# Kernel tuning notes

Hardware: AMD Instinct MI355X
Metric: run time of the kernel (lower is better)

## Reference

```python
import jax, jax.numpy as jnp
import numpy as np

BN_EPS = 1e-5


def setup_inputs() -> dict:
    key = jax.random.key(0)
    ks = jax.random.split(key, 12)
    N, K, C_IN, C_OUT = 50000, 16, 128, 128
    C2 = 2 * C_OUT
    return {
        "features": jax.random.normal(ks[0], (N, C_IN), dtype=jnp.float32),
        "neighbor_idx": jax.random.randint(ks[1], (N, K), 0, N, dtype=jnp.int64),
        "W1": jax.random.normal(ks[2], (C_IN, C2), dtype=jnp.float32) * 0.05,
        "b1": jax.random.normal(ks[3], (C2,), dtype=jnp.float32) * 0.05,
        "gamma": jax.random.uniform(ks[4], (C2,), dtype=jnp.float32, minval=0.5, maxval=1.5),
        "beta": jax.random.normal(ks[5], (C2,), dtype=jnp.float32) * 0.05,
        "run_mean": jax.random.normal(ks[6], (C2,), dtype=jnp.float32) * 0.05,
        "run_var": jax.random.uniform(ks[7], (C2,), dtype=jnp.float32, minval=0.5, maxval=1.5),
        "Ws": jax.random.normal(ks[8], (C2, C2), dtype=jnp.float32) * 0.05,
        "Wm": jax.random.normal(ks[9], (C2, C_OUT), dtype=jnp.float32) * 0.05,
        "bm": jax.random.normal(ks[10], (C_OUT,), dtype=jnp.float32) * 0.05,
    }


def reference(features, neighbor_idx, W1, b1, gamma, beta, run_mean, run_var, Ws, Wm, bm):
    # mlp1: Linear + ReLU (no BN)
    x = jax.nn.relu(features @ W1 + b1)                     # (N, 2C)
    # gather_neighbour: irregular index_select
    g = x[neighbor_idx]                                     # (N, k, 2C)
    # BatchNorm1d over channel dim (inference semantics, running stats)
    inv = gamma * jax.lax.rsqrt(run_var + BN_EPS)
    g = (g - run_mean) * inv + beta                         # (N, k, 2C)
    # AttentivePooling: per-neighbor score linear (no bias), softmax over k
    scores = jax.nn.softmax(g @ Ws, axis=1)                 # (N, k, 2C)
    feat = jnp.sum(scores * g, axis=1)                      # (N, 2C)
    return feat @ Wm + bm                                   # (N, C_out)
```

## Files before the change

kernel.cpp:

```cpp
#include <hip/hip_runtime.h>
#include <cstddef>

#define C_IN  128
#define C2    256
#define C_OUT 128
#define KNBR  16

typedef unsigned short u16;
typedef __attribute__((ext_vector_type(8))) short bf16x8;
typedef __attribute__((ext_vector_type(8))) unsigned short u16x8;
typedef __attribute__((ext_vector_type(4))) float f32x4;

__device__ __forceinline__ float bf2f(u16 h) {
    return __uint_as_float(((unsigned int)h) << 16);
}
__device__ __forceinline__ u16 f2bf(float x) {
    unsigned int u = __float_as_uint(x);
    return (u16)((u + 0x7fffu + ((u >> 16) & 1u)) >> 16);
}

__global__ void prep_k(const float* __restrict__ W1, const float* __restrict__ Ws,
                       const float* __restrict__ Wm, u16* __restrict__ W1t,
                       u16* __restrict__ Wst, u16* __restrict__ Wmt)
{
    const int n = blockIdx.x, t = threadIdx.x;
    if (blockIdx.y == 0) {
        if (t < 128) W1t[n * 128 + t] = f2bf(W1[t * 256 + n]);
    } else if (blockIdx.y == 1) {
        Wst[n * 256 + t] = f2bf(Ws[t * 256 + n]);
    } else {
        if (n < 128) Wmt[n * 256 + t] = f2bf(Wm[t * 128 + n]);
    }
}


__global__ __launch_bounds__(256)
void mlp_k(const float* __restrict__ F, const u16* __restrict__ W1t,
           const u16* __restrict__ Wst,
           const float* __restrict__ bias, const float* __restrict__ gamma,
           const float* __restrict__ beta, const float* __restrict__ mean,
           const float* __restrict__ var,
           u16* __restrict__ packed, int N)
{
    __shared__ u16 As[64][136];
    __shared__ u16 Bs[128][72];
    __shared__ u16 xs[64][264];

    const int tid = threadIdx.x;
    const int w = tid >> 6, l = tid & 63, q = l >> 4, r = l & 15;
    const int wm = w & 1, wn = w >> 1;
    const int m0 = blockIdx.x * 64;

    #pragma unroll
    for (int i = 0; i < 8; i++) {
        int idx = tid + i * 256;
        int row = idx >> 5, c4 = (idx & 31) * 4;
        int gm = m0 + row;
        float4 v = make_float4(0.f, 0.f, 0.f, 0.f);
        if (gm < N) v = *(const float4*)(F + (size_t)gm * C_IN + c4);
        ushort4 h;
        h.x = f2bf(v.x); h.y = f2bf(v.y); h.z = f2bf(v.z); h.w = f2bf(v.w);
        *(ushort4*)&As[row][c4] = h;
    }

    #pragma unroll
    for (int nh = 0; nh < 2; nh++) {
        f32x4 acc[2][4] = {};
        #pragma unroll 1
        for (int k0 = 0; k0 < C_IN; k0 += 64) {
            __syncthreads();
            #pragma unroll
            for (int i = 0; i < 4; i++) {
                int idx = tid + i * 256;
                int row = idx >> 3, g = (idx & 7) * 8;
                *(uint4*)&Bs[row][g] = *(const uint4*)(
                    W1t + (size_t)(nh * 128 + row) * C_IN + k0 + g);
            }
            __syncthreads();
            #pragma unroll
            for (int h = 0; h < 2; h++) {
                bf16x8 af[2], bfr[4];
                #pragma unroll
                for (int i = 0; i < 2; i++)
                    af[i] = *(const bf16x8*)&As[wm * 32 + i * 16 + r][k0 + h * 32 + q * 8];
                #pragma unroll
                for (int j = 0; j < 4; j++)
                    bfr[j] = *(const bf16x8*)&Bs[wn * 64 + j * 16 + r][h * 32 + q * 8];
                #pragma unroll
                for (int i = 0; i < 2; i++)
                    #pragma unroll
                    for (int j = 0; j < 4; j++)
                        acc[i][j] = __builtin_amdgcn_mfma_f32_16x16x32_bf16(
                            af[i], bfr[j], acc[i][j], 0, 0, 0);
            }
        }
        #pragma unroll
        for (int j = 0; j < 4; j++) {
            const int ch = nh * 128 + wn * 64 + j * 16 + r;
            const float bi = bias[ch], be = beta[ch], mu = mean[ch];
            const float iv = gamma[ch] * rsqrtf(var[ch] + 1e-5f);
            #pragma unroll
            for (int i = 0; i < 2; i++) {
                const int mb = wm * 32 + i * 16 + q * 4;
                #pragma unroll
                for (int p = 0; p < 4; p++) {
                    float x = fmaxf(acc[i][j][p] + bi, 0.f);
                    x = (x - mu) * iv + be;
                    xs[mb + p][ch] = f2bf(x);
                }
            }
        }
    }
    __syncthreads();

    #pragma unroll
    for (int nh = 0; nh < 2; nh++) {
        f32x4 acc[2][4] = {};
        #pragma unroll 1
        for (int k0 = 0; k0 < C2; k0 += 64) {
            __syncthreads();
            #pragma unroll
            for (int i = 0; i < 4; i++) {
                int idx = tid + i * 256;
                int row = idx >> 3, g = (idx & 7) * 8;
                *(uint4*)&Bs[row][g] = *(const uint4*)(
                    Wst + (size_t)(nh * 128 + row) * C2 + k0 + g);
            }
            __syncthreads();
            #pragma unroll
            for (int h = 0; h < 2; h++) {
                bf16x8 af[2], bfr[4];
                #pragma unroll
                for (int i = 0; i < 2; i++)
                    af[i] = *(const bf16x8*)&xs[wm * 32 + i * 16 + r][k0 + h * 32 + q * 8];
                #pragma unroll
                for (int j = 0; j < 4; j++)
                    bfr[j] = *(const bf16x8*)&Bs[wn * 64 + j * 16 + r][h * 32 + q * 8];
                #pragma unroll
                for (int i = 0; i < 2; i++)
                    #pragma unroll
                    for (int j = 0; j < 4; j++)
                        acc[i][j] = __builtin_amdgcn_mfma_f32_16x16x32_bf16(
                            af[i], bfr[j], acc[i][j], 0, 0, 0);
            }
        }
        __syncthreads();
        #pragma unroll
        for (int j = 0; j < 4; j++) {
            const int chl = wn * 64 + j * 16 + r;
            #pragma unroll
            for (int i = 0; i < 2; i++) {
                const int mb = wm * 32 + i * 16 + q * 4;
                #pragma unroll
                for (int p = 0; p < 4; p++)
                    As[mb + p][chl] = f2bf(__expf(acc[i][j][p]));
            }
        }
        __syncthreads();
        #pragma unroll
        for (int i = 0; i < 8; i++) {
            int idx = tid + i * 256;
            int row = idx >> 5, slot = idx & 31;
            int c0 = slot * 4;
            if (m0 + row < N) {
                ushort4 e  = *(const ushort4*)&As[row][c0];
                ushort4 xv = *(const ushort4*)&xs[row][nh * 128 + c0];
                uint4 qv;
                qv.x = (unsigned)e.x | ((unsigned)xv.x << 16);
                qv.y = (unsigned)e.y | ((unsigned)xv.y << 16);
                qv.z = (unsigned)e.z | ((unsigned)xv.z << 16);
                qv.w = (unsigned)e.w | ((unsigned)xv.w << 16);
                *(uint4*)(packed + (size_t)(m0 + row) * 512 + nh * 256 + slot * 8) = qv;
            }
        }
    }
}

__global__ __launch_bounds__(256)
void out_gemm(const u16* A, const u16* __restrict__ Bt,
              const float* __restrict__ bias, float* Cf, int N)
{
    __shared__ u16 As[64][72];
    __shared__ u16 Bs[128][72];
    __shared__ float STF[64][132];
    const int tid = threadIdx.x;
    const int w = tid >> 6, l = tid & 63, q = l >> 4, r = l & 15;
    const int wm = w & 1, wn = w >> 1;
    const int m0 = blockIdx.x * 64;

    f32x4 acc[2][4] = {};

    #pragma unroll 1
    for (int k0 = 0; k0 < C2; k0 += 64) {
        __syncthreads();
        #pragma unroll
        for (int i = 0; i < 2; i++) {
            int idx = tid + i * 256;
            int row = idx >> 3, g = (idx & 7) * 8;
            int gm = m0 + row;
            uint4 v = make_uint4(0u, 0u, 0u, 0u);
            if (gm < N) v = *(const uint4*)(A + (size_t)gm * C2 + k0 + g);
            *(uint4*)&As[row][g] = v;
        }
        #pragma unroll
        for (int i = 0; i < 4; i++) {
            int idx = tid + i * 256;
            int row = idx >> 3, g = (idx & 7) * 8;
            *(uint4*)&Bs[row][g] = *(const uint4*)(
                Bt + (size_t)row * C2 + k0 + g);
        }
        __syncthreads();
        #pragma unroll
        for (int h = 0; h < 2; h++) {
            bf16x8 af[2], bfr[4];
            #pragma unroll
            for (int i = 0; i < 2; i++)
                af[i] = *(const bf16x8*)&As[wm * 32 + i * 16 + r][h * 32 + q * 8];
            #pragma unroll
            for (int j = 0; j < 4; j++)
                bfr[j] = *(const bf16x8*)&Bs[wn * 64 + j * 16 + r][h * 32 + q * 8];
            #pragma unroll
            for (int i = 0; i < 2; i++)
                #pragma unroll
                for (int j = 0; j < 4; j++)
                    acc[i][j] = __builtin_amdgcn_mfma_f32_16x16x32_bf16(
                        af[i], bfr[j], acc[i][j], 0, 0, 0);
        }
    }
    __syncthreads();

    #pragma unroll
    for (int j = 0; j < 4; j++) {
        const int ch = wn * 64 + j * 16 + r;
        const float bo = bias[ch];
        #pragma unroll
        for (int i = 0; i < 2; i++) {
            const int mb = wm * 32 + i * 16 + q * 4;
            #pragma unroll
            for (int p = 0; p < 4; p++)
                STF[mb + p][ch] = acc[i][j][p] + bo;
        }
    }
    __syncthreads();
    #pragma unroll
    for (int i = 0; i < 8; i++) {
        int idx = tid + i * 256;
        int row = idx >> 5, c4 = (idx & 31) * 4;
        if (m0 + row < N)
            *(float4*)(Cf + (size_t)(m0 + row) * C_OUT + c4) =
                *(const float4*)&STF[row][c4];
    }
}

__global__ __launch_bounds__(256)
void gather_k(const u16* __restrict__ packed, const int* __restrict__ nidx,
              u16* __restrict__ featb, int N)
{
    __shared__ int rows[4 * KNBR];
    const int tid = threadIdx.x;
    const int p0 = blockIdx.x * 4;

    if (tid < 4 * KNBR) {
        int n = p0 + (tid >> 4);
        rows[tid] = (n < N) ? nidx[n * KNBR + (tid & 15)] : 0;
    }
    __syncthreads();

    const int w = tid >> 6;
    const int l = tid & 63;
    const int p = p0 + w;
    if (p >= N) return;

    u16x8 v[KNBR];
    #pragma unroll
    for (int k = 0; k < KNBR; k++)
        v[k] = *(const u16x8*)(packed + (size_t)rows[w * KNBR + k] * 512 + l * 8);

    float num[4] = {0.f, 0.f, 0.f, 0.f};
    float den[4] = {0.f, 0.f, 0.f, 0.f};
    #pragma unroll
    for (int k = 0; k < KNBR; k++) {
        #pragma unroll
        for (int c = 0; c < 4; c++) {
            float e = bf2f((u16)v[k][2 * c]);
            float x = bf2f((u16)v[k][2 * c + 1]);
            den[c] += e;
            num[c] = fmaf(e, x, num[c]);
        }
    }
    ushort4 o;
    o.x = f2bf(num[0] / den[0]); o.y = f2bf(num[1] / den[1]);
    o.z = f2bf(num[2] / den[2]); o.w = f2bf(num[3] / den[3]);
    *(ushort4*)(featb + (size_t)p * C2 + l * 4) = o;
}

extern "C" void kernel_launch(void* const* d_in, const int* in_sizes, int n_in,
                              void* d_out, int out_size, void* d_ws, size_t ws_size,
                              hipStream_t stream)
{
    const float* features = (const float*)d_in[0];
    const int*   nidx     = (const int*)d_in[1];
    const float* W1       = (const float*)d_in[2];
    const float* b1       = (const float*)d_in[3];
    const float* gamma    = (const float*)d_in[4];
    const float* beta     = (const float*)d_in[5];
    const float* mean     = (const float*)d_in[6];
    const float* var      = (const float*)d_in[7];
    const float* Ws       = (const float*)d_in[8];
    const float* Wm       = (const float*)d_in[9];
    const float* bm       = (const float*)d_in[10];
    float* out = (float*)d_out;

    const int N = in_sizes[0] / C_IN;

    u16* packed = (u16*)d_ws;
    u16* W1t    = packed + (size_t)N * 512;
    u16* Wst    = W1t + 256 * 128;
    u16* Wmt    = Wst + 256 * 256;
    u16* featb = (u16*)d_out;

    prep_k<<<dim3(256, 3), 256, 0, stream>>>(W1, Ws, Wm, W1t, Wst, Wmt);

    const int MT = (N + 63) / 64;

    mlp_k<<<MT, 256, 0, stream>>>(features, W1t, Wst, b1, gamma, beta,
                                  mean, var, packed, N);
    gather_k<<<(N + 3) / 4, 256, 0, stream>>>(packed, nidx, featb, N);
    out_gemm<<<MT, 256, 0, stream>>>(featb, Wmt, bm, out, N);
}
```

Baseline: 256.8 us.

## Fuse neighbor gather-pooling with output GEMM into one kernel

Merges the gather/softmax-pooling kernel and the output projection GEMM into one kernel that processes 32 points per block. The pooled features stay in shared memory as the GEMM A-tile, so the intermediate bf16 buffer is never written to and re-read from global memory, and one launch is removed. In exchange, each block reloads the full Wm tile for only 32 rows, and the gather phase runs as a serial per-wave loop before the MFMA phase, which may reduce latency hiding.

```diff
diff --git a/kernel.cpp b/kernel.cpp
--- a/kernel.cpp
+++ b/kernel.cpp
@@ -5,6 +5,7 @@
 #define C2    256
 #define C_OUT 128
 #define KNBR  16
+#define PTS   32
 
 typedef unsigned short u16;
 typedef __attribute__((ext_vector_type(8))) short bf16x8;
@@ -177,31 +178,58 @@
 }
 
 __global__ __launch_bounds__(256)
-void out_gemm(const u16* A, const u16* __restrict__ Bt,
-              const float* __restrict__ bias, float* Cf, int N)
+void gather_out_k(const u16* __restrict__ packed, const int* __restrict__ nidx,
+                  const u16* __restrict__ Bt, const float* __restrict__ bias,
+                  float* __restrict__ Cf, int N)
 {
-    __shared__ u16 As[64][72];
+    __shared__ int rows[PTS * KNBR];
     __shared__ u16 Bs[128][72];
-    __shared__ float STF[64][132];
+    __shared__ __align__(16) u16 fsm[PTS * 264];
+
     const int tid = threadIdx.x;
     const int w = tid >> 6, l = tid & 63, q = l >> 4, r = l & 15;
+    const int m0 = blockIdx.x * PTS;
+
+    #pragma unroll
+    for (int i = 0; i < 2; i++) {
+        int idx = tid + i * 256;
+        int n = m0 + (idx >> 4);
+        rows[idx] = (n < N) ? nidx[n * KNBR + (idx & 15)] : 0;
+    }
+    __syncthreads();
+
+    #pragma unroll 1
+    for (int ip = 0; ip < 8; ip++) {
+        const int pl = w * 8 + ip;
+        u16x8 v[KNBR];
+        #pragma unroll
+        for (int k = 0; k < KNBR; k++)
+            v[k] = *(const u16x8*)(packed + (size_t)rows[pl * KNBR + k] * 512 + l * 8);
+        float num[4] = {0.f, 0.f, 0.f, 0.f};
+        float den[4] = {0.f, 0.f, 0.f, 0.f};
+        #pragma unroll
+        for (int k = 0; k < KNBR; k++) {
+            #pragma unroll
+            for (int c = 0; c < 4; c++) {
+                float e = bf2f((u16)v[k][2 * c]);
+                float x = bf2f((u16)v[k][2 * c + 1]);
+                den[c] += e;
+                num[c] = fmaf(e, x, num[c]);
+            }
+        }
+        ushort4 o;
+        o.x = f2bf(num[0] / den[0]); o.y = f2bf(num[1] / den[1]);
+        o.z = f2bf(num[2] / den[2]); o.w = f2bf(num[3] / den[3]);
+        *(ushort4*)&fsm[pl * 264 + l * 4] = o;
+    }
+    __syncthreads();
+
     const int wm = w & 1, wn = w >> 1;
-    const int m0 = blockIdx.x * 64;
-
-    f32x4 acc[2][4] = {};
+    f32x4 acc[4] = {};
 
     #pragma unroll 1
     for (int k0 = 0; k0 < C2; k0 += 64) {
         __syncthreads();
-        #pragma unroll
-        for (int i = 0; i < 2; i++) {
-            int idx = tid + i * 256;
-            int row = idx >> 3, g = (idx & 7) * 8;
-            int gm = m0 + row;
-            uint4 v = make_uint4(0u, 0u, 0u, 0u);
-            if (gm < N) v = *(const uint4*)(A + (size_t)gm * C2 + k0 + g);
-            *(uint4*)&As[row][g] = v;
-        }
         #pragma unroll
         for (int i = 0; i < 4; i++) {
             int idx = tid + i * 256;
@@ -212,86 +240,38 @@
         __syncthreads();
         #pragma unroll
         for (int h = 0; h < 2; h++) {
-            bf16x8 af[2], bfr[4];
-            #pragma unroll
-            for (int i = 0; i < 2; i++)
-                af[i] = *(const bf16x8*)&As[wm * 32 + i * 16 + r][h * 32 + q * 8];
+            bf16x8 af, bfr[4];
+            af = *(const bf16x8*)&fsm[(wm * 16 + r) * 264 + k0 + h * 32 + q * 8];
             #pragma unroll
             for (int j = 0; j < 4; j++)
                 bfr[j] = *(const bf16x8*)&Bs[wn * 64 + j * 16 + r][h * 32 + q * 8];
             #pragma unroll
-            for (int i = 0; i < 2; i++)
-                #pragma unroll
-                for (int j = 0; j < 4; j++)
-                    acc[i][j] = __builtin_amdgcn_mfma_f32_16x16x32_bf16(
-                        af[i], bfr[j], acc[i][j], 0, 0, 0);
-        }
-    }
-    __syncthreads();
-
+            for (int j = 0; j < 4; j++)
+                acc[j] = __builtin_amdgcn_mfma_f32_16x16x32_bf16(
+                    af, bfr[j], acc[j], 0, 0, 0);
+        }
+    }
+    __syncthreads();
+
+    float* STF = (float*)fsm;
     #pragma unroll
     for (int j = 0; j < 4; j++) {
         const int ch = wn * 64 + j * 16 + r;
         const float bo = bias[ch];
-        #pragma unroll
-        for (int i = 0; i < 2; i++) {
-            const int mb = wm * 32 + i * 16 + q * 4;
-            #pragma unroll
-            for (int p = 0; p < 4; p++)
-                STF[mb + p][ch] = acc[i][j][p] + bo;
-        }
-    }
-    __syncthreads();
-    #pragma unroll
-    for (int i = 0; i < 8; i++) {
+        const int mb = wm * 16 + q * 4;
+        #pragma unroll
+        for (int p = 0; p < 4; p++)
+            STF[(mb + p) * 132 + ch] = acc[j][p] + bo;
+    }
+    __syncthreads();
+    #pragma unroll
+    for (int i = 0; i < 4; i++) {
         int idx = tid + i * 256;
         int row = idx >> 5, c4 = (idx & 31) * 4;
         if (m0 + row < N)
             *(float4*)(Cf + (size_t)(m0 + row) * C_OUT + c4) =
-                *(const float4*)&STF[row][c4];
-    }
-}
-
-__global__ __launch_bounds__(256)
-void gather_k(const u16* __restrict__ packed, const int* __restrict__ nidx,
-              u16* __restrict__ featb, int N)
-{
-    __shared__ int rows[4 * KNBR];
-    const int tid = threadIdx.x;
-    const int p0 = blockIdx.x * 4;
-
-    if (tid < 4 * KNBR) {
-        int n = p0 + (tid >> 4);
-        rows[tid] = (n < N) ? nidx[n * KNBR + (tid & 15)] : 0;
-    }
-    __syncthreads();
-
-    const int w = tid >> 6;
-    const int l = tid & 63;
-    const int p = p0 + w;
-    if (p >= N) return;
-
-    u16x8 v[KNBR];
-    #pragma unroll
-    for (int k = 0; k < KNBR; k++)
-        v[k] = *(const u16x8*)(packed + (size_t)rows[w * KNBR + k] * 512 + l * 8);
-
-    float num[4] = {0.f, 0.f, 0.f, 0.f};
-    float den[4] = {0.f, 0.f, 0.f, 0.f};
-    #pragma unroll
-    for (int k = 0; k < KNBR; k++) {
-        #pragma unroll
-        for (int c = 0; c < 4; c++) {
-            float e = bf2f((u16)v[k][2 * c]);
-            float x = bf2f((u16)v[k][2 * c + 1]);
-            den[c] += e;
-            num[c] = fmaf(e, x, num[c]);
-        }
-    }
-    ushort4 o;
-    o.x = f2bf(num[0] / den[0]); o.y = f2bf(num[1] / den[1]);
-    o.z = f2bf(num[2] / den[2]); o.w = f2bf(num[3] / den[3]);
-    *(ushort4*)(featb + (size_t)p * C2 + l * 4) = o;
+                *(const float4*)&STF[row * 132 + c4];
+    }
 }
 
 extern "C" void kernel_launch(void* const* d_in, const int* in_sizes, int n_in,
@@ -317,14 +297,13 @@
     u16* W1t    = packed + (size_t)N * 512;
     u16* Wst    = W1t + 256 * 128;
     u16* Wmt    = Wst + 256 * 256;
-    u16* featb = (u16*)d_out;
 
     prep_k<<<dim3(256, 3), 256, 0, stream>>>(W1, Ws, Wm, W1t, Wst, Wmt);
 
     const int MT = (N + 63) / 64;
+    const int GT = (N + PTS - 1) / PTS;
 
     mlp_k<<<MT, 256, 0, stream>>>(features, W1t, Wst, b1, gamma, beta,
                                   mean, var, packed, N);
-    gather_k<<<(N + 3) / 4, 256, 0, stream>>>(packed, nidx, featb, N);
-    out_gemm<<<MT, 256, 0, stream>>>(featb, Wmt, bm, out, N);
-}
+    gather_out_k<<<GT, 256, 0, stream>>>(packed, nidx, Wmt, bm, out, N);
+}
```

After: 255.0 us. No clear change (-0.7%).
